# Kernel tuning notes

Hardware: AMD Instinct MI355X
Metric: run time of the kernel (lower is better)

The kernel has to match this reference:

```python
import jax, jax.numpy as jnp
import numpy as np

B, S, D = 2, 2048, 768
H = 12
DH = D // H
EPS = 1e-12


def setup_inputs() -> dict:
    key = jax.random.key(0)
    ks = jax.random.split(key, 16)
    s = 0.02
    return {
        "hidden_states": jax.random.normal(ks[0], (B, S, D), jnp.float32),
        "attention_mask": jnp.zeros((B, 1, 1, S), jnp.float32),
        "position_bias": jax.random.normal(ks[1], (1, H, S, S), jnp.float32),
        "q_w": jax.random.normal(ks[2], (D, D), jnp.float32) * s,
        "q_b": jnp.zeros((D,), jnp.float32),
        "k_w": jax.random.normal(ks[3], (D, D), jnp.float32) * s,
        "k_b": jnp.zeros((D,), jnp.float32),
        "v_w": jax.random.normal(ks[4], (D, D), jnp.float32) * s,
        "v_b": jnp.zeros((D,), jnp.float32),
        "o_w": jax.random.normal(ks[5], (D, D), jnp.float32) * s,
        "o_b": jnp.zeros((D,), jnp.float32),
        "ln_w": jnp.ones((D,), jnp.float32),
        "ln_b": jnp.zeros((D,), jnp.float32),
    }


def _split_heads(x):
    # [B, S, D] -> [B, H, S, DH]
    b, s, _ = x.shape
    return x.reshape(b, s, H, DH).transpose(0, 2, 1, 3)


def reference(hidden_states, attention_mask, position_bias,
              q_w, q_b, k_w, k_b, v_w, v_b, o_w, o_b, ln_w, ln_b):
    # nn.Linear: y = x @ W.T + b (W stored [out, in])
    q = _split_heads(hidden_states @ q_w.T + q_b)
    k = _split_heads(hidden_states @ k_w.T + k_b)
    v = _split_heads(hidden_states @ v_w.T + v_b)

    scale = 1.0 / jnp.sqrt(jnp.asarray(DH, hidden_states.dtype))
    scores = jnp.einsum('bhqd,bhkd->bhqk', q, k) * scale
    scores = scores + position_bias + attention_mask
    probs = jax.nn.softmax(scores, axis=-1)

    c = jnp.einsum('bhqk,bhkd->bhqd', probs, v)
    c = c.transpose(0, 2, 1, 3).reshape(hidden_states.shape[0], -1, D)
    o = c @ o_w.T + o_b

    # residual + LayerNorm (dropout is identity at eval)
    x = o + hidden_states
    mu = jnp.mean(x, axis=-1, keepdims=True)
    var = jnp.mean(jnp.square(x - mu), axis=-1, keepdims=True)
    out = (x - mu) * jax.lax.rsqrt(var + EPS) * ln_w + ln_b
    return out
```

## Files before the change

kernel.cpp:

```cpp
#include <hip/hip_runtime.h>
#include <math.h>

typedef unsigned short u16;
typedef float f32x4 __attribute__((ext_vector_type(4)));
typedef __bf16 bf16x8 __attribute__((ext_vector_type(8)));

#define B_ 2
#define S_ 2048
#define D_ 768
#define H_ 12
#define DH_ 64

__device__ __forceinline__ u16 f2bf(float x) {
  union { float f; unsigned u; } v; v.f = x;
  unsigned r = v.u + 0x7fffu + ((v.u >> 16) & 1u);
  return (u16)(r >> 16);
}

__device__ __forceinline__ f32x4 zero4() { f32x4 z = {0.f, 0.f, 0.f, 0.f}; return z; }

__device__ __forceinline__ f32x4 mfma16(bf16x8 a, bf16x8 b, f32x4 c) {
  return __builtin_amdgcn_mfma_f32_16x16x32_bf16(a, b, c, 0, 0, 0);
}

__device__ __forceinline__ void gload_lds16(const void* g, void* l) {
  __builtin_amdgcn_global_load_lds((const __attribute__((address_space(1))) void*)g,
                                   (__attribute__((address_space(3))) void*)l, 16, 0, 0);
}

__global__ void cvt_kernel(const float* __restrict__ hid, const float* __restrict__ qw,
                           const float* __restrict__ kw, const float* __restrict__ vw,
                           const float* __restrict__ ow, u16* __restrict__ Hb,
                           u16* __restrict__ Wb) {
  const int NH = B_ * S_ * D_;
  const int NW = D_ * D_;
  const int T4 = (NH + 4 * NW) >> 2;
  int stride = gridDim.x * blockDim.x;
  for (int i = blockIdx.x * blockDim.x + threadIdx.x; i < T4; i += stride) {
    int e = i << 2;
    const float* src; u16* dst;
    if (e < NH) { src = hid + e; dst = Hb + e; }
    else {
      int o = e - NH;
      int m = o / NW, oo = o - m * NW;
      src = (m == 0 ? qw : m == 1 ? kw : m == 2 ? vw : ow) + oo;
      dst = Wb + o;
    }
    f32x4 v = *(const f32x4*)src;
    uint2 o2;
    o2.x = (unsigned)f2bf(v[0]) | ((unsigned)f2bf(v[1]) << 16);
    o2.y = (unsigned)f2bf(v[2]) | ((unsigned)f2bf(v[3]) << 16);
    *(uint2*)dst = o2;
  }
}

#define BM 128
#define BN 128
#define BK 64

__global__ __launch_bounds__(256) void gemm_kernel(
    const u16* __restrict__ A, const u16* __restrict__ W,
    const float* __restrict__ bq, const float* __restrict__ bk, const float* __restrict__ bv,
    u16* __restrict__ Qb, u16* __restrict__ Kb, u16* __restrict__ Vtmp,
    float* __restrict__ Of, const float* __restrict__ bO, int mode)
{
  __shared__ __align__(16) u16 As[BM * BK];
  __shared__ __align__(16) u16 Bs[BN * BK];
  int t = threadIdx.x;
  int lane = t & 63, w = t >> 6;
  int wr = w >> 1, wc = w & 1;
  int l15 = lane & 15, l4 = lane >> 4;
  int m0 = blockIdx.y * BM, n0 = blockIdx.x * BN;

  f32x4 acc[4][4];
#pragma unroll
  for (int i = 0; i < 4; ++i)
#pragma unroll
    for (int j = 0; j < 4; ++j) acc[i][j] = zero4();

  const int K = D_;
  for (int k0 = 0; k0 < K; k0 += BK) {
    __syncthreads();
#pragma unroll
    for (int p = 0; p < 4; ++p) {
      int seg = p * 4 + w;
      int bd = seg * 64 + lane;
      int row = bd >> 3;
      int slot = (bd & 7) ^ (row & 7);
      gload_lds16(A + (size_t)(m0 + row) * K + k0 + slot * 8, (char*)As + seg * 1024);
      gload_lds16(W + (size_t)(n0 + row) * K + k0 + slot * 8, (char*)Bs + seg * 1024);
    }
    __syncthreads();
#pragma unroll
    for (int kk = 0; kk < 2; ++kk) {
      bf16x8 af[4], bfr[4];
#pragma unroll
      for (int i = 0; i < 4; ++i) {
        int ra = wr * 64 + i * 16 + l15;
        af[i] = *(const bf16x8*)((const char*)As + ra * 128 +
                                 ((kk * 64 + (l4 << 4)) ^ ((ra & 7) << 4)));
        int rb = wc * 64 + i * 16 + l15;
        bfr[i] = *(const bf16x8*)((const char*)Bs + rb * 128 +
                                  ((kk * 64 + (l4 << 4)) ^ ((rb & 7) << 4)));
      }
#pragma unroll
      for (int i = 0; i < 4; ++i)
#pragma unroll
        for (int j = 0; j < 4; ++j)
          acc[i][j] = mfma16(af[i], bfr[j], acc[i][j]);
    }
  }

  if (mode == 0) {
    int mat = n0 / D_;
    int ncol0 = (n0 - mat * D_) + wc * 64;
    const float* bias = (mat == 0) ? bq : (mat == 1 ? bk : bv);
    u16* outp = (mat == 0) ? Qb : (mat == 1 ? Kb : Vtmp);
    float scale = (mat == 0) ? 0.125f : 1.0f;
    int h = ncol0 >> 6;
#pragma unroll
    for (int j = 0; j < 4; ++j) {
      int d = j * 16 + l15;
      float bvv = bias[ncol0 + d];
#pragma unroll
      for (int i = 0; i < 4; ++i) {
#pragma unroll
        for (int r = 0; r < 4; ++r) {
          int m = m0 + wr * 64 + i * 16 + (l4 << 2) + r;
          int bb = m >> 11, ss = m & 2047;
          float val = (acc[i][j][r] + bvv) * scale;
          outp[(((size_t)bb * H_ + h) * S_ + ss) * DH_ + d] = f2bf(val);
        }
      }
    }
  } else {
#pragma unroll
    for (int j = 0; j < 4; ++j) {
      int n = n0 + wc * 64 + j * 16 + l15;
      float bvv = bO[n];
#pragma unroll
      for (int i = 0; i < 4; ++i) {
#pragma unroll
        for (int r = 0; r < 4; ++r) {
          int m = m0 + wr * 64 + i * 16 + (l4 << 2) + r;
          Of[(size_t)m * D_ + n] = acc[i][j][r] + bvv;
        }
      }
    }
  }
}

__global__ __launch_bounds__(256) void vtrans_kernel(const u16* __restrict__ V,
                                                     u16* __restrict__ Vt) {
  __shared__ __align__(16) u16 tile[64 * 64];
  int t = threadIdx.x;
  int s0 = blockIdx.x * 64;
  int bh = blockIdx.y;
  const u16* src = V + ((size_t)bh * S_ + s0) * DH_;
#pragma unroll
  for (int p = 0; p < 2; ++p) {
    int bd = t + p * 256;
    int row = bd >> 3, slot = bd & 7;
    uint4 v = *(const uint4*)(src + row * 64 + slot * 8);
    *(uint4*)((char*)tile + row * 128 + ((slot ^ (row & 7)) << 4)) = v;
  }
  __syncthreads();
  int d = t >> 2, sc = (t & 3) * 16;
  u16* dst = Vt + ((size_t)bh * DH_ + d) * S_ + s0 + sc;
  int colB = d * 2;
#pragma unroll
  for (int half = 0; half < 2; ++half) {
    u16 tmp[8] __attribute__((aligned(16)));
#pragma unroll
    for (int j = 0; j < 8; ++j) {
      int s = sc + half * 8 + j;
      tmp[j] = *(const u16*)((const char*)tile + s * 128 +
                             (((colB >> 4) ^ (s & 7)) << 4) + (colB & 15));
    }
    *(uint4*)(dst + half * 8) = *(const uint4*)tmp;
  }
}

__global__ __launch_bounds__(256) void attn_kernel(
    const u16* __restrict__ Qb, const u16* __restrict__ Kb, const u16* __restrict__ Vt,
    const float* __restrict__ bias, const float* __restrict__ mask, u16* __restrict__ Cb)
{
  __shared__ __align__(16) u16 Ks[2][64 * 64];
  __shared__ __align__(16) u16 Vs[2][64 * 64];
  __shared__ __align__(16) u16 Ps[4][16][72];
  int t = threadIdx.x, lane = t & 63, w = t >> 6;
  int q0 = blockIdx.x * 64, h = blockIdx.y, b = blockIdx.z;
  size_t bh = (size_t)b * H_ + h;
  const u16* Qp = Qb + (bh * S_ + q0) * DH_;
  const u16* Kp = Kb + bh * S_ * DH_;
  const u16* Vp = Vt + bh * DH_ * S_;
  const float* biasp = bias + ((size_t)h * S_ + q0) * S_;
  const float* maskp = mask + (size_t)b * S_;
  int l15 = lane & 15, l4 = lane >> 4;

  const float* brp0 = biasp + (size_t)(w * 16 + (l4 << 2) + 0) * S_ + l15;
  const float* brp1 = brp0 + S_;
  const float* brp2 = brp1 + S_;
  const float* brp3 = brp2 + S_;

  bf16x8 qf0, qf1;
  {
    const u16* qrow = Qp + (w * 16 + l15) * DH_;
    qf0 = *(const bf16x8*)(qrow + l4 * 8);
    qf1 = *(const bf16x8*)(qrow + 32 + l4 * 8);
  }

  f32x4 oacc[4];
#pragma unroll
  for (int i = 0; i < 4; ++i) oacc[i] = zero4();
  float lrow[4] = {0.f, 0.f, 0.f, 0.f};

  float bc0[4], bc1[4], bc2[4], bc3[4];
  float bn0[4], bn1[4], bn2[4], bn3[4];

#pragma unroll
  for (int p = 0; p < 2; ++p) {
    int seg = p * 4 + w;
    int bd = seg * 64 + lane;
    int row = bd >> 3;
    int slot = (bd & 7) ^ (row & 7);
    gload_lds16(Kp + (size_t)row * DH_ + slot * 8, (char*)Ks[0] + seg * 1024);
    gload_lds16(Vp + (size_t)row * S_ + slot * 8, (char*)Vs[0] + seg * 1024);
  }
#pragma unroll
  for (int kf = 0; kf < 4; ++kf) {
    float mk = maskp[kf * 16 + l15];
    bc0[kf] = brp0[kf * 16] + mk;
    bc1[kf] = brp1[kf * 16] + mk;
    bc2[kf] = brp2[kf * 16] + mk;
    bc3[kf] = brp3[kf * 16] + mk;
  }
  __syncthreads();

  int cur = 0;
  for (int kt = 0; kt < S_ / 64; ++kt) {
    int k0 = kt * 64;
    if (kt + 1 < S_ / 64) {
      int k0n = k0 + 64;
      const u16* Kn = Kp + (size_t)k0n * DH_;
#pragma unroll
      for (int p = 0; p < 2; ++p) {
        int seg = p * 4 + w;
        int bd = seg * 64 + lane;
        int row = bd >> 3;
        int slot = (bd & 7) ^ (row & 7);
        gload_lds16(Kn + (size_t)row * DH_ + slot * 8, (char*)Ks[cur ^ 1] + seg * 1024);
        gload_lds16(Vp + (size_t)row * S_ + k0n + slot * 8, (char*)Vs[cur ^ 1] + seg * 1024);
      }
#pragma unroll
      for (int kf = 0; kf < 4; ++kf) {
        float mk = maskp[k0n + kf * 16 + l15];
        bn0[kf] = brp0[k0n + kf * 16] + mk;
        bn1[kf] = brp1[k0n + kf * 16] + mk;
        bn2[kf] = brp2[k0n + kf * 16] + mk;
        bn3[kf] = brp3[k0n + kf * 16] + mk;
      }
    }

    const u16* Kc = Ks[cur];
    const u16* Vc = Vs[cur];

    f32x4 sf[4];
#pragma unroll
    for (int kf = 0; kf < 4; ++kf) {
      int row = kf * 16 + l15;
      bf16x8 kb0 = *(const bf16x8*)((const char*)Kc + row * 128 +
                                    ((l4 << 4) ^ ((row & 7) << 4)));
      bf16x8 kb1 = *(const bf16x8*)((const char*)Kc + row * 128 +
                                    ((64 + (l4 << 4)) ^ ((row & 7) << 4)));
      f32x4 s0 = zero4();
      s0 = mfma16(qf0, kb0, s0);
      s0 = mfma16(qf1, kb1, s0);
      sf[kf] = s0;
    }

#pragma unroll
    for (int kf = 0; kf < 4; ++kf) {
      float p0 = __expf(sf[kf][0] + bc0[kf]);
      float p1 = __expf(sf[kf][1] + bc1[kf]);
      float p2 = __expf(sf[kf][2] + bc2[kf]);
      float p3 = __expf(sf[kf][3] + bc3[kf]);
      sf[kf][0] = p0; sf[kf][1] = p1; sf[kf][2] = p2; sf[kf][3] = p3;
      lrow[0] += p0; lrow[1] += p1; lrow[2] += p2; lrow[3] += p3;
    }

#pragma unroll
    for (int r = 0; r < 4; ++r)
#pragma unroll
      for (int kf = 0; kf < 4; ++kf)
        Ps[w][(l4 << 2) + r][kf * 16 + l15] = f2bf(sf[kf][r]);

    bf16x8 pa0 = *(const bf16x8*)&Ps[w][l15][l4 * 8];
    bf16x8 pa1 = *(const bf16x8*)&Ps[w][l15][32 + l4 * 8];

#pragma unroll
    for (int df = 0; df < 4; ++df) {
      int row = df * 16 + l15;
      bf16x8 vb0 = *(const bf16x8*)((const char*)Vc + row * 128 +
                                    ((l4 << 4) ^ ((row & 7) << 4)));
      bf16x8 vb1 = *(const bf16x8*)((const char*)Vc + row * 128 +
                                    ((64 + (l4 << 4)) ^ ((row & 7) << 4)));
      oacc[df] = mfma16(pa0, vb0, oacc[df]);
      oacc[df] = mfma16(pa1, vb1, oacc[df]);
    }

    __syncthreads();
    cur ^= 1;
#pragma unroll
    for (int kf = 0; kf < 4; ++kf) {
      bc0[kf] = bn0[kf]; bc1[kf] = bn1[kf];
      bc2[kf] = bn2[kf]; bc3[kf] = bn3[kf];
    }
  }

#pragma unroll
  for (int r = 0; r < 4; ++r) {
    float ls = lrow[r];
#pragma unroll
    for (int o = 1; o < 16; o <<= 1) ls += __shfl_xor(ls, o, 64);
    float inv = 1.0f / ls;
    int q = q0 + w * 16 + (l4 << 2) + r;
    size_t base = ((size_t)b * S_ + q) * D_ + h * DH_ + l15;
#pragma unroll
    for (int df = 0; df < 4; ++df)
      Cb[base + df * 16] = f2bf(oacc[df][r] * inv);
  }
}

__global__ __launch_bounds__(192) void ln_kernel(const float* __restrict__ O,
                                                 const float* __restrict__ hid,
                                                 const float* __restrict__ lw,
                                                 const float* __restrict__ lb,
                                                 float* __restrict__ out) {
  int row = blockIdx.x, t = threadIdx.x;
  size_t base = (size_t)row * D_;
  f32x4 x = *(const f32x4*)(O + base + t * 4);
  f32x4 hh = *(const f32x4*)(hid + base + t * 4);
  x = x + hh;
  float s = x[0] + x[1] + x[2] + x[3];
  float s2 = x[0] * x[0] + x[1] * x[1] + x[2] * x[2] + x[3] * x[3];
#pragma unroll
  for (int o = 1; o < 64; o <<= 1) {
    s += __shfl_xor(s, o, 64);
    s2 += __shfl_xor(s2, o, 64);
  }
  __shared__ float rs[3], rs2[3];
  int w = t >> 6, lane = t & 63;
  if (lane == 0) { rs[w] = s; rs2[w] = s2; }
  __syncthreads();
  s = rs[0] + rs[1] + rs[2];
  s2 = rs2[0] + rs2[1] + rs2[2];
  float mu = s * (1.0f / 768.0f);
  float var = s2 * (1.0f / 768.0f) - mu * mu;
  float rstd = rsqrtf(var + 1e-12f);
  f32x4 w4 = *(const f32x4*)(lw + t * 4);
  f32x4 b4 = *(const f32x4*)(lb + t * 4);
  f32x4 y = (x - mu) * rstd * w4 + b4;
  *(f32x4*)(out + base + t * 4) = y;
}

extern "C" void kernel_launch(void* const* d_in, const int* in_sizes, int n_in,
                              void* d_out, int out_size, void* d_ws, size_t ws_size,
                              hipStream_t stream) {
  const float* hid  = (const float*)d_in[0];
  const float* mask = (const float*)d_in[1];
  const float* bias = (const float*)d_in[2];
  const float* qw = (const float*)d_in[3];
  const float* qb = (const float*)d_in[4];
  const float* kw = (const float*)d_in[5];
  const float* kb = (const float*)d_in[6];
  const float* vw = (const float*)d_in[7];
  const float* vb = (const float*)d_in[8];
  const float* ow = (const float*)d_in[9];
  const float* ob = (const float*)d_in[10];
  const float* lnw = (const float*)d_in[11];
  const float* lnb = (const float*)d_in[12];

  char* ws = (char*)d_ws;
  const size_t NHB = (size_t)B_ * S_ * D_ * 2;
  const size_t NWB = (size_t)4 * D_ * D_ * 2;
  const size_t NQB = (size_t)B_ * H_ * S_ * DH_ * 2;
  u16* Hb = (u16*)ws;
  u16* Wb = (u16*)(ws + NHB);
  u16* Qb = (u16*)(ws + NHB + NWB);
  u16* Kb = (u16*)(ws + NHB + NWB + NQB);
  u16* Vt = (u16*)(ws + NHB + NWB + 2 * NQB);
  u16* Cb = (u16*)(ws + NHB + NWB + 3 * NQB);
  float* Of = (float*)(ws + NHB + NWB + 4 * NQB);
  u16* Vtmp = (u16*)Of;

  cvt_kernel<<<2048, 256, 0, stream>>>(hid, qw, kw, vw, ow, Hb, Wb);

  gemm_kernel<<<dim3(18, 32), 256, 0, stream>>>(
      Hb, Wb, qb, kb, vb, Qb, Kb, Vtmp, nullptr, nullptr, 0);

  vtrans_kernel<<<dim3(S_ / 64, B_ * H_), 256, 0, stream>>>(Vtmp, Vt);

  attn_kernel<<<dim3(S_ / 64, H_, B_), 256, 0, stream>>>(Qb, Kb, Vt, bias, mask, Cb);

  gemm_kernel<<<dim3(6, 32), 256, 0, stream>>>(
      Cb, Wb + (size_t)3 * D_ * D_, nullptr, nullptr, nullptr,
      nullptr, nullptr, nullptr, Of, ob, 1);

  ln_kernel<<<B_ * S_, 192, 0, stream>>>(Of, hid, lnw, lnb, (float*)d_out);
}
```

Baseline: 154.1 us.

## Split attention key tile across two wave groups with LDS reduction of partial outputs

The attention kernel now runs 8 waves per block. Four query-row groups are each split across two key halves, so every wave handles 32 of the 64 keys per tile, and the K/V tile loads are spread over 512 threads. At the end, the partial row sums and output accumulators from the second key group pass through a shared-memory pool aliased with the P buffer and are combined by the first group before normalising and storing. This aims to raise wave-level parallelism and latency hiding, at the cost of a final reduction, more LDS and more barrier participants.

```diff
diff --git a/kernel.cpp b/kernel.cpp
--- a/kernel.cpp
+++ b/kernel.cpp
@@ -181,14 +181,19 @@
   }
 }
 
-__global__ __launch_bounds__(256) void attn_kernel(
+__global__ __launch_bounds__(512, 6) void attn_kernel(
     const u16* __restrict__ Qb, const u16* __restrict__ Kb, const u16* __restrict__ Vt,
     const float* __restrict__ bias, const float* __restrict__ mask, u16* __restrict__ Cb)
 {
   __shared__ __align__(16) u16 Ks[2][64 * 64];
   __shared__ __align__(16) u16 Vs[2][64 * 64];
-  __shared__ __align__(16) u16 Ps[4][16][72];
+  __shared__ __align__(16) char upool[17408];
+  u16 (*Ps)[16][72] = (u16 (*)[16][72])upool;
+  float (*Osh)[16][66] = (float (*)[16][66])upool;
+  float (*Lsh)[2][16] = (float (*)[2][16])(upool + 16896);
+
   int t = threadIdx.x, lane = t & 63, w = t >> 6;
+  int qg = w & 3, kg = w >> 2;
   int q0 = blockIdx.x * 64, h = blockIdx.y, b = blockIdx.z;
   size_t bh = (size_t)b * H_ + h;
   const u16* Qp = Qb + (bh * S_ + q0) * DH_;
@@ -197,15 +202,17 @@
   const float* biasp = bias + ((size_t)h * S_ + q0) * S_;
   const float* maskp = mask + (size_t)b * S_;
   int l15 = lane & 15, l4 = lane >> 4;
-
-  const float* brp0 = biasp + (size_t)(w * 16 + (l4 << 2) + 0) * S_ + l15;
+  int kc0 = kg * 32;
+
+  const float* brp0 = biasp + (size_t)(qg * 16 + (l4 << 2) + 0) * S_ + kc0 + l15;
   const float* brp1 = brp0 + S_;
   const float* brp2 = brp1 + S_;
   const float* brp3 = brp2 + S_;
+  const float* mkp = maskp + kc0 + l15;
 
   bf16x8 qf0, qf1;
   {
-    const u16* qrow = Qp + (w * 16 + l15) * DH_;
+    const u16* qrow = Qp + (qg * 16 + l15) * DH_;
     qf0 = *(const bf16x8*)(qrow + l4 * 8);
     qf1 = *(const bf16x8*)(qrow + 32 + l4 * 8);
   }
@@ -215,21 +222,18 @@
   for (int i = 0; i < 4; ++i) oacc[i] = zero4();
   float lrow[4] = {0.f, 0.f, 0.f, 0.f};
 
-  float bc0[4], bc1[4], bc2[4], bc3[4];
-  float bn0[4], bn1[4], bn2[4], bn3[4];
-
-#pragma unroll
-  for (int p = 0; p < 2; ++p) {
-    int seg = p * 4 + w;
-    int bd = seg * 64 + lane;
-    int row = bd >> 3;
-    int slot = (bd & 7) ^ (row & 7);
-    gload_lds16(Kp + (size_t)row * DH_ + slot * 8, (char*)Ks[0] + seg * 1024);
-    gload_lds16(Vp + (size_t)row * S_ + slot * 8, (char*)Vs[0] + seg * 1024);
-  }
-#pragma unroll
-  for (int kf = 0; kf < 4; ++kf) {
-    float mk = maskp[kf * 16 + l15];
+  float bc0[2], bc1[2], bc2[2], bc3[2];
+  float bn0[2], bn1[2], bn2[2], bn3[2];
+
+  {
+    int row = t >> 3;
+    int slot = (t & 7) ^ (row & 7);
+    gload_lds16(Kp + (size_t)row * DH_ + slot * 8, (char*)Ks[0] + w * 1024);
+    gload_lds16(Vp + (size_t)row * S_ + slot * 8, (char*)Vs[0] + w * 1024);
+  }
+#pragma unroll
+  for (int kf = 0; kf < 2; ++kf) {
+    float mk = mkp[kf * 16];
     bc0[kf] = brp0[kf * 16] + mk;
     bc1[kf] = brp1[kf * 16] + mk;
     bc2[kf] = brp2[kf * 16] + mk;
@@ -242,19 +246,13 @@
     int k0 = kt * 64;
     if (kt + 1 < S_ / 64) {
       int k0n = k0 + 64;
-      const u16* Kn = Kp + (size_t)k0n * DH_;
-#pragma unroll
-      for (int p = 0; p < 2; ++p) {
-        int seg = p * 4 + w;
-        int bd = seg * 64 + lane;
-        int row = bd >> 3;
-        int slot = (bd & 7) ^ (row & 7);
-        gload_lds16(Kn + (size_t)row * DH_ + slot * 8, (char*)Ks[cur ^ 1] + seg * 1024);
-        gload_lds16(Vp + (size_t)row * S_ + k0n + slot * 8, (char*)Vs[cur ^ 1] + seg * 1024);
-      }
-#pragma unroll
-      for (int kf = 0; kf < 4; ++kf) {
-        float mk = maskp[k0n + kf * 16 + l15];
+      int row = t >> 3;
+      int slot = (t & 7) ^ (row & 7);
+      gload_lds16(Kp + (size_t)(k0n + row) * DH_ + slot * 8, (char*)Ks[cur ^ 1] + w * 1024);
+      gload_lds16(Vp + (size_t)row * S_ + k0n + slot * 8, (char*)Vs[cur ^ 1] + w * 1024);
+#pragma unroll
+      for (int kf = 0; kf < 2; ++kf) {
+        float mk = mkp[k0n + kf * 16];
         bn0[kf] = brp0[k0n + kf * 16] + mk;
         bn1[kf] = brp1[k0n + kf * 16] + mk;
         bn2[kf] = brp2[k0n + kf * 16] + mk;
@@ -265,10 +263,10 @@
     const u16* Kc = Ks[cur];
     const u16* Vc = Vs[cur];
 
-    f32x4 sf[4];
-#pragma unroll
-    for (int kf = 0; kf < 4; ++kf) {
-      int row = kf * 16 + l15;
+    f32x4 sf[2];
+#pragma unroll
+    for (int kf = 0; kf < 2; ++kf) {
+      int row = kc0 + kf * 16 + l15;
       bf16x8 kb0 = *(const bf16x8*)((const char*)Kc + row * 128 +
                                     ((l4 << 4) ^ ((row & 7) << 4)));
       bf16x8 kb1 = *(const bf16x8*)((const char*)Kc + row * 128 +
@@ -280,7 +278,7 @@
     }
 
 #pragma unroll
-    for (int kf = 0; kf < 4; ++kf) {
+    for (int kf = 0; kf < 2; ++kf) {
       float p0 = __expf(sf[kf][0] + bc0[kf]);
       float p1 = __expf(sf[kf][1] + bc1[kf]);
       float p2 = __expf(sf[kf][2] + bc2[kf]);
@@ -292,27 +290,23 @@
 #pragma unroll
     for (int r = 0; r < 4; ++r)
 #pragma unroll
-      for (int kf = 0; kf < 4; ++kf)
-        Ps[w][(l4 << 2) + r][kf * 16 + l15] = f2bf(sf[kf][r]);
-
-    bf16x8 pa0 = *(const bf16x8*)&Ps[w][l15][l4 * 8];
-    bf16x8 pa1 = *(const bf16x8*)&Ps[w][l15][32 + l4 * 8];
+      for (int kf = 0; kf < 2; ++kf)
+        Ps[qg][(l4 << 2) + r][kc0 + kf * 16 + l15] = f2bf(sf[kf][r]);
+
+    bf16x8 pa = *(const bf16x8*)&Ps[qg][l15][kc0 + l4 * 8];
 
 #pragma unroll
     for (int df = 0; df < 4; ++df) {
       int row = df * 16 + l15;
-      bf16x8 vb0 = *(const bf16x8*)((const char*)Vc + row * 128 +
-                                    ((l4 << 4) ^ ((row & 7) << 4)));
-      bf16x8 vb1 = *(const bf16x8*)((const char*)Vc + row * 128 +
-                                    ((64 + (l4 << 4)) ^ ((row & 7) << 4)));
-      oacc[df] = mfma16(pa0, vb0, oacc[df]);
-      oacc[df] = mfma16(pa1, vb1, oacc[df]);
+      bf16x8 vb = *(const bf16x8*)((const char*)Vc + row * 128 +
+                                   ((kg * 64 + (l4 << 4)) ^ ((row & 7) << 4)));
+      oacc[df] = mfma16(pa, vb, oacc[df]);
     }
 
     __syncthreads();
     cur ^= 1;
 #pragma unroll
-    for (int kf = 0; kf < 4; ++kf) {
+    for (int kf = 0; kf < 2; ++kf) {
       bc0[kf] = bn0[kf]; bc1[kf] = bn1[kf];
       bc2[kf] = bn2[kf]; bc3[kf] = bn3[kf];
     }
@@ -320,15 +314,32 @@
 
 #pragma unroll
   for (int r = 0; r < 4; ++r) {
-    float ls = lrow[r];
-#pragma unroll
-    for (int o = 1; o < 16; o <<= 1) ls += __shfl_xor(ls, o, 64);
-    float inv = 1.0f / ls;
-    int q = q0 + w * 16 + (l4 << 2) + r;
-    size_t base = ((size_t)b * S_ + q) * D_ + h * DH_ + l15;
-#pragma unroll
-    for (int df = 0; df < 4; ++df)
-      Cb[base + df * 16] = f2bf(oacc[df][r] * inv);
+#pragma unroll
+    for (int o = 1; o < 16; o <<= 1) lrow[r] += __shfl_xor(lrow[r], o, 64);
+  }
+  if (l15 == 0) {
+#pragma unroll
+    for (int r = 0; r < 4; ++r) Lsh[qg][kg][(l4 << 2) + r] = lrow[r];
+  }
+  if (kg == 1) {
+#pragma unroll
+    for (int r = 0; r < 4; ++r)
+#pragma unroll
+      for (int df = 0; df < 4; ++df)
+        Osh[qg][(l4 << 2) + r][df * 16 + l15] = oacc[df][r];
+  }
+  __syncthreads();
+  if (kg == 0) {
+#pragma unroll
+    for (int r = 0; r < 4; ++r) {
+      int rr = (l4 << 2) + r;
+      float inv = 1.0f / (Lsh[qg][0][rr] + Lsh[qg][1][rr]);
+      int q = q0 + qg * 16 + rr;
+      size_t base = ((size_t)b * S_ + q) * D_ + h * DH_ + l15;
+#pragma unroll
+      for (int df = 0; df < 4; ++df)
+        Cb[base + df * 16] = f2bf((oacc[df][r] + Osh[qg][rr][df * 16 + l15]) * inv);
+    }
   }
 }
 
@@ -401,7 +412,7 @@
 
   vtrans_kernel<<<dim3(S_ / 64, B_ * H_), 256, 0, stream>>>(Vtmp, Vt);
 
-  attn_kernel<<<dim3(S_ / 64, H_, B_), 256, 0, stream>>>(Qb, Kb, Vt, bias, mask, Cb);
+  attn_kernel<<<dim3(S_ / 64, H_, B_), 512, 0, stream>>>(Qb, Kb, Vt, bias, mask, Cb);
 
   gemm_kernel<<<dim3(6, 32), 256, 0, stream>>>(
       Cb, Wb + (size_t)3 * D_ * D_, nullptr, nullptr, nullptr,
```

New measurement: 149.8 us. -2.8%, faster.

## Merge both batches into one 512-thread attention block to share position-bias reads

Applied to the files above, without the earlier changes.

The attention kernel now launches one 512-thread block per (query tile, head) and handles both batch elements in it. Even waves take batch 0 and odd waves batch 1, and each block loads K/V tiles for both batches into the two LDS buffers. The goal is better cache reuse of the large position_bias tensor, which is shared across batches, and half as many blocks. In exchange the K/V double buffering is dropped: loads are issued at the top of each iteration and waited on by a barrier, so global latency is no longer hidden behind compute.

```diff
diff --git a/kernel.cpp b/kernel.cpp
--- a/kernel.cpp
+++ b/kernel.cpp
@@ -181,31 +181,40 @@
   }
 }
 
-__global__ __launch_bounds__(256) void attn_kernel(
+__global__ __launch_bounds__(512, 4) void attn_kernel(
     const u16* __restrict__ Qb, const u16* __restrict__ Kb, const u16* __restrict__ Vt,
     const float* __restrict__ bias, const float* __restrict__ mask, u16* __restrict__ Cb)
 {
   __shared__ __align__(16) u16 Ks[2][64 * 64];
   __shared__ __align__(16) u16 Vs[2][64 * 64];
-  __shared__ __align__(16) u16 Ps[4][16][72];
+  __shared__ __align__(16) u16 Ps[8][16][72];
+
   int t = threadIdx.x, lane = t & 63, w = t >> 6;
-  int q0 = blockIdx.x * 64, h = blockIdx.y, b = blockIdx.z;
+  int b = w & 1, qg = w >> 1;
+  int q0 = blockIdx.x * 64, h = blockIdx.y;
+  int l15 = lane & 15, l4 = lane >> 4;
+
+  const float* biasp = bias + ((size_t)h * S_ + q0) * S_;
+  const float* maskp = mask + (size_t)b * S_;
   size_t bh = (size_t)b * H_ + h;
   const u16* Qp = Qb + (bh * S_ + q0) * DH_;
-  const u16* Kp = Kb + bh * S_ * DH_;
-  const u16* Vp = Vt + bh * DH_ * S_;
-  const float* biasp = bias + ((size_t)h * S_ + q0) * S_;
-  const float* maskp = mask + (size_t)b * S_;
-  int l15 = lane & 15, l4 = lane >> 4;
-
-  const float* brp0 = biasp + (size_t)(w * 16 + (l4 << 2) + 0) * S_ + l15;
+
+  const float* brp0 = biasp + (size_t)(qg * 16 + (l4 << 2) + 0) * S_ + l15;
   const float* brp1 = brp0 + S_;
   const float* brp2 = brp1 + S_;
   const float* brp3 = brp2 + S_;
+  const float* mkp = maskp + l15;
+
+  int srow = t >> 3;
+  int sslot = (t & 7) ^ (srow & 7);
+  const u16* gK0 = Kb + (((size_t)0 * H_ + h) * S_ + srow) * DH_ + sslot * 8;
+  const u16* gK1 = Kb + (((size_t)1 * H_ + h) * S_ + srow) * DH_ + sslot * 8;
+  const u16* gV0 = Vt + (((size_t)0 * H_ + h) * DH_ + srow) * S_ + sslot * 8;
+  const u16* gV1 = Vt + (((size_t)1 * H_ + h) * DH_ + srow) * S_ + sslot * 8;
 
   bf16x8 qf0, qf1;
   {
-    const u16* qrow = Qp + (w * 16 + l15) * DH_;
+    const u16* qrow = Qp + (qg * 16 + l15) * DH_;
     qf0 = *(const bf16x8*)(qrow + l4 * 8);
     qf1 = *(const bf16x8*)(qrow + 32 + l4 * 8);
   }
@@ -219,51 +228,39 @@
   float bn0[4], bn1[4], bn2[4], bn3[4];
 
 #pragma unroll
-  for (int p = 0; p < 2; ++p) {
-    int seg = p * 4 + w;
-    int bd = seg * 64 + lane;
-    int row = bd >> 3;
-    int slot = (bd & 7) ^ (row & 7);
-    gload_lds16(Kp + (size_t)row * DH_ + slot * 8, (char*)Ks[0] + seg * 1024);
-    gload_lds16(Vp + (size_t)row * S_ + slot * 8, (char*)Vs[0] + seg * 1024);
-  }
-#pragma unroll
   for (int kf = 0; kf < 4; ++kf) {
-    float mk = maskp[kf * 16 + l15];
+    float mk = mkp[kf * 16];
     bc0[kf] = brp0[kf * 16] + mk;
     bc1[kf] = brp1[kf * 16] + mk;
     bc2[kf] = brp2[kf * 16] + mk;
     bc3[kf] = brp3[kf * 16] + mk;
   }
-  __syncthreads();
-
-  int cur = 0;
+
   for (int kt = 0; kt < S_ / 64; ++kt) {
-    int k0 = kt * 64;
+    {
+      size_t ko = (size_t)kt * 64 * DH_;
+      size_t vo = (size_t)kt * 64;
+      gload_lds16(gK0 + ko, (char*)Ks[0] + w * 1024);
+      gload_lds16(gK1 + ko, (char*)Ks[1] + w * 1024);
+      gload_lds16(gV0 + vo, (char*)Vs[0] + w * 1024);
+      gload_lds16(gV1 + vo, (char*)Vs[1] + w * 1024);
+    }
+    __syncthreads();
+
     if (kt + 1 < S_ / 64) {
-      int k0n = k0 + 64;
-      const u16* Kn = Kp + (size_t)k0n * DH_;
-#pragma unroll
-      for (int p = 0; p < 2; ++p) {
-        int seg = p * 4 + w;
-        int bd = seg * 64 + lane;
-        int row = bd >> 3;
-        int slot = (bd & 7) ^ (row & 7);
-        gload_lds16(Kn + (size_t)row * DH_ + slot * 8, (char*)Ks[cur ^ 1] + seg * 1024);
-        gload_lds16(Vp + (size_t)row * S_ + k0n + slot * 8, (char*)Vs[cur ^ 1] + seg * 1024);
+      int kb = (kt + 1) * 64;
+#pragma unroll
+      for (int kf = 0; kf < 4; ++kf) {
+        float mk = mkp[kb + kf * 16];
+        bn0[kf] = brp0[kb + kf * 16] + mk;
+        bn1[kf] = brp1[kb + kf * 16] + mk;
+        bn2[kf] = brp2[kb + kf * 16] + mk;
+        bn3[kf] = brp3[kb + kf * 16] + mk;
       }
-#pragma unroll
-      for (int kf = 0; kf < 4; ++kf) {
-        float mk = maskp[k0n + kf * 16 + l15];
-        bn0[kf] = brp0[k0n + kf * 16] + mk;
-        bn1[kf] = brp1[k0n + kf * 16] + mk;
-        bn2[kf] = brp2[k0n + kf * 16] + mk;
-        bn3[kf] = brp3[k0n + kf * 16] + mk;
-      }
-    }
-
-    const u16* Kc = Ks[cur];
-    const u16* Vc = Vs[cur];
+    }
+
+    const u16* Kc = Ks[b];
+    const u16* Vc = Vs[b];
 
     f32x4 sf[4];
 #pragma unroll
@@ -310,7 +307,6 @@
     }
 
     __syncthreads();
-    cur ^= 1;
 #pragma unroll
     for (int kf = 0; kf < 4; ++kf) {
       bc0[kf] = bn0[kf]; bc1[kf] = bn1[kf];
@@ -324,7 +320,7 @@
 #pragma unroll
     for (int o = 1; o < 16; o <<= 1) ls += __shfl_xor(ls, o, 64);
     float inv = 1.0f / ls;
-    int q = q0 + w * 16 + (l4 << 2) + r;
+    int q = q0 + qg * 16 + (l4 << 2) + r;
     size_t base = ((size_t)b * S_ + q) * D_ + h * DH_ + l15;
 #pragma unroll
     for (int df = 0; df < 4; ++df)
@@ -401,7 +397,7 @@
 
   vtrans_kernel<<<dim3(S_ / 64, B_ * H_), 256, 0, stream>>>(Vtmp, Vt);
 
-  attn_kernel<<<dim3(S_ / 64, H_, B_), 256, 0, stream>>>(Qb, Kb, Vt, bias, mask, Cb);
+  attn_kernel<<<dim3(S_ / 64, H_), 512, 0, stream>>>(Qb, Kb, Vt, bias, mask, Cb);
 
   gemm_kernel<<<dim3(6, 32), 256, 0, stream>>>(
       Cb, Wb + (size_t)3 * D_ * D_, nullptr, nullptr, nullptr,
```

Result: slower. 159.5 us (+3.5%).
